# Optimization experiments

Hardware: AMD Instinct MI355X
Metric: run time of the kernel (lower is better)

## Reference

```python
import jax, jax.numpy as jnp
import numpy as np

NEG = -1e6  # masked_softmax fill value from the torch source


def setup_inputs() -> dict:
    key = jax.random.key(0)
    ks = jax.random.split(key, 7)
    B, NQ, NK, D, H = 4, 256, 1024, 256, 256
    queries = jax.random.normal(ks[0], (B, NQ, D), dtype=jnp.float32)
    keys_ = jax.random.normal(ks[1], (B, NK, D), dtype=jnp.float32)
    values = jax.random.normal(ks[2], (B, NK, D), dtype=jnp.float32)
    valid_lens = jax.random.randint(ks[3], (B,), 1, NK + 1, dtype=jnp.int32)
    scale = 1.0 / np.sqrt(D)
    Wq = jax.random.normal(ks[4], (D, H), dtype=jnp.float32) * scale
    Wk = jax.random.normal(ks[5], (D, H), dtype=jnp.float32) * scale
    w_v = jax.random.normal(ks[6], (H,), dtype=jnp.float32) * (1.0 / np.sqrt(H))
    return {"queries": queries, "keys": keys_, "values": values,
            "valid_lens": valid_lens, "Wq": Wq, "Wk": Wk, "w_v": w_v}


def reference(queries, keys, values, valid_lens, Wq, Wk, w_v):
    # projections
    q = jnp.einsum('bqd,dh->bqh', queries, Wq)           # [B,NQ,H]
    k = jnp.einsum('bkd,dh->bkh', keys, Wk)              # [B,NK,H]
    # broadcast-add + tanh + dense(->1): scores [B,NQ,NK]
    features = jnp.tanh(q[:, :, None, :] + k[:, None, :, :])  # [B,NQ,NK,H]
    scores = jnp.einsum('bqkh,h->bqk', features, w_v)
    # masked softmax over last axis with per-batch valid lengths
    nk = keys.shape[1]
    mask = jnp.arange(nk)[None, None, :] < valid_lens[:, None, None]  # [B,1,NK]
    scores = jnp.where(mask, scores, NEG)
    attn = jax.nn.softmax(scores, axis=-1)               # [B,NQ,NK]
    # dropout in eval mode -> identity
    return jnp.einsum('bqk,bkd->bqd', attn, values)      # [B,NQ,D]
```

## Files before the change

### kernel.cpp

```cpp
#include <hip/hip_runtime.h>
#include <math.h>

#define BB 4
#define NQ 256
#define NK 1024
#define DD 256
#define HH 256

#define TM 64
#define TN 64
#define TKK 16
#define NT (DD / TKK)

__global__ __launch_bounds__(256) void proj_exp_kernel(
    const float* __restrict__ Q, const float* __restrict__ K,
    const float* __restrict__ Wq, const float* __restrict__ Wk,
    const int* __restrict__ vlen,
    float* __restrict__ Eq, float* __restrict__ Ek)
{
    const int QTILES = (BB * NQ) / TM;
    int bx = blockIdx.x;
    const float* A; const float* W; float* C; int bm;
    if (bx < QTILES) { A = Q; W = Wq; C = Eq; bm = bx * TM; }
    else {
        int kt = bx - QTILES;
        int b = kt >> 4;
        int lr = (kt & 15) * TM;
        if (lr >= vlen[b]) return;
        A = K; W = Wk; C = Ek; bm = kt * TM;
    }
    int bn = blockIdx.y * TN;

    __shared__ float As[2][TKK][TM + 4];
    __shared__ float Ws[2][TKK][TN + 4];

    int tid = threadIdx.x;
    int ar = tid >> 2, ac4 = tid & 3;
    int wkk = tid >> 4, wc4 = tid & 15;
    int ty = tid >> 4, tx = tid & 15;

    float4 aR = *(const float4*)&A[(size_t)(bm + ar) * DD + ac4 * 4];
    float4 wR = *(const float4*)&W[(size_t)wkk * HH + bn + wc4 * 4];

    float acc[4][4] = {};

    for (int t = 0; t < NT; ++t) {
        int cur = t & 1;
        As[cur][ac4 * 4 + 0][ar] = aR.x;
        As[cur][ac4 * 4 + 1][ar] = aR.y;
        As[cur][ac4 * 4 + 2][ar] = aR.z;
        As[cur][ac4 * 4 + 3][ar] = aR.w;
        *(float4*)&Ws[cur][wkk][wc4 * 4] = wR;
        if (t + 1 < NT) {
            int k0 = (t + 1) * TKK;
            aR = *(const float4*)&A[(size_t)(bm + ar) * DD + k0 + ac4 * 4];
            wR = *(const float4*)&W[(size_t)(k0 + wkk) * HH + bn + wc4 * 4];
        }
        __syncthreads();
#pragma unroll
        for (int kk = 0; kk < TKK; ++kk) {
            float4 a4 = *(const float4*)&As[cur][kk][ty * 4];
            float4 w4 = *(const float4*)&Ws[cur][kk][tx * 4];
            acc[0][0] = fmaf(a4.x, w4.x, acc[0][0]);
            acc[0][1] = fmaf(a4.x, w4.y, acc[0][1]);
            acc[0][2] = fmaf(a4.x, w4.z, acc[0][2]);
            acc[0][3] = fmaf(a4.x, w4.w, acc[0][3]);
            acc[1][0] = fmaf(a4.y, w4.x, acc[1][0]);
            acc[1][1] = fmaf(a4.y, w4.y, acc[1][1]);
            acc[1][2] = fmaf(a4.y, w4.z, acc[1][2]);
            acc[1][3] = fmaf(a4.y, w4.w, acc[1][3]);
            acc[2][0] = fmaf(a4.z, w4.x, acc[2][0]);
            acc[2][1] = fmaf(a4.z, w4.y, acc[2][1]);
            acc[2][2] = fmaf(a4.z, w4.z, acc[2][2]);
            acc[2][3] = fmaf(a4.z, w4.w, acc[2][3]);
            acc[3][0] = fmaf(a4.w, w4.x, acc[3][0]);
            acc[3][1] = fmaf(a4.w, w4.y, acc[3][1]);
            acc[3][2] = fmaf(a4.w, w4.z, acc[3][2]);
            acc[3][3] = fmaf(a4.w, w4.w, acc[3][3]);
        }
        __syncthreads();
    }

#pragma unroll
    for (int i = 0; i < 4; ++i) {
        int m = bm + ty * 4 + i;
        float4 o;
        o.x = __expf(2.f * fminf(fmaxf(acc[i][0], -8.f), 8.f));
        o.y = __expf(2.f * fminf(fmaxf(acc[i][1], -8.f), 8.f));
        o.z = __expf(2.f * fminf(fmaxf(acc[i][2], -8.f), 8.f));
        o.w = __expf(2.f * fminf(fmaxf(acc[i][3], -8.f), 8.f));
        *(float4*)&C[(size_t)m * HH + bn + tx * 4] = o;
    }
}

__global__ __launch_bounds__(256) void scores_kernel(
    const float* __restrict__ Eq, const float* __restrict__ Ek,
    const float* __restrict__ wv, const int* __restrict__ vlen,
    float* __restrict__ P, float* __restrict__ Psum)
{
    __shared__ __align__(16) float sQ[32][HH + 4];
    __shared__ __align__(16) float sK[32][HH + 4];
    __shared__ __align__(16) float sW[HH];

    int bid = blockIdx.x;
    int b = bid & 3;
    int rest = bid >> 2;
    int qc = rest & 7;
    int kc = rest >> 3;
    int L = vlen[b];
    int k0 = kc * 32;
    if (k0 >= L) return;
    int q0 = qc * 32;

    int tid = threadIdx.x;
    {
        int c4 = tid & 63, r0 = tid >> 6;
        const float4* gq = (const float4*)(Eq + ((size_t)b * NQ + q0) * HH);
        const float4* gk = (const float4*)(Ek + ((size_t)b * NK + k0) * HH);
#pragma unroll
        for (int r = 0; r < 32; r += 4) {
            *(float4*)&sQ[r + r0][c4 * 4] = gq[(size_t)(r + r0) * (HH / 4) + c4];
            *(float4*)&sK[r + r0][c4 * 4] = gk[(size_t)(r + r0) * (HH / 4) + c4];
        }
        sW[tid] = wv[tid];
    }
    __syncthreads();

    int ki = tid & 15, qi = tid >> 4;
    float a00 = 0.f, a01 = 0.f, a10 = 0.f, a11 = 0.f;
    const float4* qp0 = (const float4*)&sQ[qi][0];
    const float4* qp1 = (const float4*)&sQ[qi + 16][0];
    const float4* kp0 = (const float4*)&sK[ki][0];
    const float4* kp1 = (const float4*)&sK[ki + 16][0];
    const float4* wp  = (const float4*)sW;

#pragma unroll 4
    for (int h4 = 0; h4 < HH / 4; ++h4) {
        float4 w = wp[h4];
        float wxy = w.x + w.y, wzw = w.z + w.w;
        float4 A0 = qp0[h4], A1 = qp1[h4];
        float4 B0 = kp0[h4], B1 = kp1[h4];
#define QUAD(acc, Aq, Bk)                                                    \
        {                                                                    \
            float E1 = Aq.x * Bk.x, E2 = Aq.y * Bk.y;                        \
            float E3 = Aq.z * Bk.z, E4 = Aq.w * Bk.w;                        \
            float d1 = E1 + 1.f, d2 = E2 + 1.f;                              \
            float d3 = E3 + 1.f, d4 = E4 + 1.f;                              \
            float n12 = fmaf(w.x, E2, fmaf(w.y, E1, wxy));                   \
            float n34 = fmaf(w.z, E4, fmaf(w.w, E3, wzw));                   \
            float d12 = d1 * d2, d34 = d3 * d4;                              \
            float num = fmaf(n12, d34, n34 * d12);                           \
            acc = fmaf(num, __builtin_amdgcn_rcpf(d12 * d34), acc);          \
        }
        QUAD(a00, A0, B0);
        QUAD(a01, A0, B1);
        QUAD(a10, A1, B0);
        QUAD(a11, A1, B1);
#undef QUAD
    }

    int kA = k0 + ki, kB = kA + 16;
    float p00 = (kA < L) ? __expf(-2.f * a00) : 0.f;
    float p10 = (kA < L) ? __expf(-2.f * a10) : 0.f;
    float p01 = (kB < L) ? __expf(-2.f * a01) : 0.f;
    float p11 = (kB < L) ? __expf(-2.f * a11) : 0.f;

    float* s0 = P + ((size_t)b * NQ + q0 + qi) * NK;
    float* s1 = P + ((size_t)b * NQ + q0 + qi + 16) * NK;
    s0[kA] = p00; s0[kB] = p01;
    s1[kA] = p10; s1[kB] = p11;

    float r0s = p00 + p01, r1s = p10 + p11;
#pragma unroll
    for (int o = 1; o <= 8; o <<= 1) {
        r0s += __shfl_xor(r0s, o, 64);
        r1s += __shfl_xor(r1s, o, 64);
    }
    if (ki == 0) {
        Psum[((size_t)b * NQ + q0 + qi) * 32 + kc] = r0s;
        Psum[((size_t)b * NQ + q0 + qi + 16) * 32 + kc] = r1s;
    }
}

__global__ __launch_bounds__(256) void pv_kernel(
    const float* __restrict__ P, const float* __restrict__ V,
    const float* __restrict__ Psum, const int* __restrict__ vlen,
    float* __restrict__ out)
{
    __shared__ __align__(16) float sPt[2][32][36];
    __shared__ __align__(16) float sV[2][32][36];
    __shared__ float sAll[3][64][17];
    __shared__ float sRowsum[32];

    int bid = blockIdx.x;
    int b = bid & 3;
    int rest = bid >> 2;
    int qt = rest >> 3, dt = rest & 7;
    int q0 = qt * 32, d0 = dt * 32;
    int L = vlen[b];
    int nc = (L + 31) >> 5;

    int tid = threadIdx.x;
    if (tid < 32) {
        float s = 0.f;
        const float* pp = Psum + ((size_t)b * NQ + q0 + tid) * 32;
        for (int c = 0; c < nc; ++c) s += pp[c];
        sRowsum[tid] = s;
    }

    int r = tid >> 3, c4 = tid & 7;
    int w = tid >> 6, sp = tid & 63;
    int qg = sp >> 3, dg = sp & 7;

    const float* Pb = P + ((size_t)b * NQ + q0 + r) * NK;
    const float* Vb = V + (size_t)b * NK * DD + d0;

    float4 pf = *(const float4*)(Pb + c4 * 4);
    float4 vf = *(const float4*)(Vb + (size_t)r * DD + c4 * 4);

    float acc[4][4] = {};

    for (int c = 0; c < nc; ++c) {
        int cur = c & 1;
        sPt[cur][c4 * 4 + 0][r] = pf.x;
        sPt[cur][c4 * 4 + 1][r] = pf.y;
        sPt[cur][c4 * 4 + 2][r] = pf.z;
        sPt[cur][c4 * 4 + 3][r] = pf.w;
        *(float4*)&sV[cur][r][c4 * 4] = vf;
        if (c + 1 < nc) {
            int kn = (c + 1) * 32;
            pf = *(const float4*)(Pb + kn + c4 * 4);
            vf = *(const float4*)(Vb + (size_t)(kn + r) * DD + c4 * 4);
        }
        __syncthreads();
#pragma unroll
        for (int kk = 0; kk < 8; ++kk) {
            float4 A  = *(const float4*)&sPt[cur][w * 8 + kk][qg * 4];
            float4 Bv = *(const float4*)&sV[cur][w * 8 + kk][dg * 4];
            acc[0][0] = fmaf(A.x, Bv.x, acc[0][0]);
            acc[0][1] = fmaf(A.x, Bv.y, acc[0][1]);
            acc[0][2] = fmaf(A.x, Bv.z, acc[0][2]);
            acc[0][3] = fmaf(A.x, Bv.w, acc[0][3]);
            acc[1][0] = fmaf(A.y, Bv.x, acc[1][0]);
            acc[1][1] = fmaf(A.y, Bv.y, acc[1][1]);
            acc[1][2] = fmaf(A.y, Bv.z, acc[1][2]);
            acc[1][3] = fmaf(A.y, Bv.w, acc[1][3]);
            acc[2][0] = fmaf(A.z, Bv.x, acc[2][0]);
            acc[2][1] = fmaf(A.z, Bv.y, acc[2][1]);
            acc[2][2] = fmaf(A.z, Bv.z, acc[2][2]);
            acc[2][3] = fmaf(A.z, Bv.w, acc[2][3]);
            acc[3][0] = fmaf(A.w, Bv.x, acc[3][0]);
            acc[3][1] = fmaf(A.w, Bv.y, acc[3][1]);
            acc[3][2] = fmaf(A.w, Bv.z, acc[3][2]);
            acc[3][3] = fmaf(A.w, Bv.w, acc[3][3]);
        }
        __syncthreads();
    }

    if (w > 0) {
#pragma unroll
        for (int i = 0; i < 4; ++i)
#pragma unroll
            for (int j = 0; j < 4; ++j) sAll[w - 1][sp][i * 4 + j] = acc[i][j];
    }
    __syncthreads();
    if (w == 0) {
#pragma unroll
        for (int ww = 0; ww < 3; ++ww)
#pragma unroll
            for (int i = 0; i < 4; ++i)
#pragma unroll
                for (int j = 0; j < 4; ++j) acc[i][j] += sAll[ww][sp][i * 4 + j];
#pragma unroll
        for (int i = 0; i < 4; ++i) {
            float inv = 1.0f / sRowsum[qg * 4 + i];
            float4 o = { acc[i][0] * inv, acc[i][1] * inv,
                         acc[i][2] * inv, acc[i][3] * inv };
            *(float4*)&out[((size_t)b * NQ + q0 + qg * 4 + i) * DD + d0 + dg * 4] = o;
        }
    }
}

extern "C" void kernel_launch(void* const* d_in, const int* in_sizes, int n_in,
                              void* d_out, int out_size, void* d_ws, size_t ws_size,
                              hipStream_t stream) {
    const float* queries = (const float*)d_in[0];
    const float* keys    = (const float*)d_in[1];
    const float* values  = (const float*)d_in[2];
    const int*   vlens   = (const int*)d_in[3];
    const float* Wq      = (const float*)d_in[4];
    const float* Wk      = (const float*)d_in[5];
    const float* wv      = (const float*)d_in[6];
    float* out = (float*)d_out;

    float* Eqb  = (float*)d_ws;
    float* Ekb  = Eqb + (size_t)BB * NQ * HH;
    float* P    = Ekb + (size_t)BB * NK * HH;
    float* Psum = P + (size_t)BB * NQ * NK;

    dim3 pgrid((BB * NQ) / TM + (BB * NK) / TM, HH / TN);
    proj_exp_kernel<<<pgrid, 256, 0, stream>>>(queries, keys, Wq, Wk, vlens,
                                               Eqb, Ekb);

    scores_kernel<<<dim3(BB * (NQ / 32) * (NK / 32)), 256, 0, stream>>>(
        Eqb, Ekb, wv, vlens, P, Psum);

    pv_kernel<<<dim3(BB * (NQ / 32) * (DD / 32)), 256, 0, stream>>>(
        P, values, Psum, vlens, out);
}
```

Before: 56.14 us.

## Stream scores-kernel H dimension in double-buffered chunks and drop trailing barriers

The scores kernel no longer stages full 256-wide Q and K rows in shared memory. It streams 64-wide H chunks through a double buffer, prefetching the next chunk into registers while the current one is computed, with a single barrier per chunk. This shrinks LDS use substantially, which should allow more resident blocks and overlap global loads with math. The trailing __syncthreads in the projection and PV GEMM loops is also removed. That saves barriers, but it could introduce shared-memory races if those loops depended on the barrier before overwriting a buffer.

```diff
diff --git a/kernel.cpp b/kernel.cpp
--- a/kernel.cpp
+++ b/kernel.cpp
@@ -78,7 +78,6 @@
             acc[3][2] = fmaf(a4.w, w4.z, acc[3][2]);
             acc[3][3] = fmaf(a4.w, w4.w, acc[3][3]);
         }
-        __syncthreads();
     }
 
 #pragma unroll
@@ -93,13 +92,16 @@
     }
 }
 
+#define HC 64
+#define NHCH (HH / HC)
+
 __global__ __launch_bounds__(256) void scores_kernel(
     const float* __restrict__ Eq, const float* __restrict__ Ek,
     const float* __restrict__ wv, const int* __restrict__ vlen,
     float* __restrict__ P, float* __restrict__ Psum)
 {
-    __shared__ __align__(16) float sQ[32][HH + 4];
-    __shared__ __align__(16) float sK[32][HH + 4];
+    __shared__ __align__(16) float sQ[2][32][HC + 4];
+    __shared__ __align__(16) float sK[2][32][HC + 4];
     __shared__ __align__(16) float sW[HH];
 
     int bid = blockIdx.x;
@@ -113,50 +115,62 @@
     int q0 = qc * 32;
 
     int tid = threadIdx.x;
-    {
-        int c4 = tid & 63, r0 = tid >> 6;
-        const float4* gq = (const float4*)(Eq + ((size_t)b * NQ + q0) * HH);
-        const float4* gk = (const float4*)(Ek + ((size_t)b * NK + k0) * HH);
-#pragma unroll
-        for (int r = 0; r < 32; r += 4) {
-            *(float4*)&sQ[r + r0][c4 * 4] = gq[(size_t)(r + r0) * (HH / 4) + c4];
-            *(float4*)&sK[r + r0][c4 * 4] = gk[(size_t)(r + r0) * (HH / 4) + c4];
-        }
-        sW[tid] = wv[tid];
-    }
-    __syncthreads();
+    int lr = tid >> 3;
+    int lc = tid & 7;
+
+    const float* gq = Eq + ((size_t)b * NQ + q0 + lr) * HH;
+    const float* gk = Ek + ((size_t)b * NK + k0 + lr) * HH;
+
+    float4 q1 = *(const float4*)&gq[lc * 4];
+    float4 q2 = *(const float4*)&gq[lc * 4 + 32];
+    float4 k1 = *(const float4*)&gk[lc * 4];
+    float4 k2 = *(const float4*)&gk[lc * 4 + 32];
+    sW[tid] = wv[tid];
 
     int ki = tid & 15, qi = tid >> 4;
     float a00 = 0.f, a01 = 0.f, a10 = 0.f, a11 = 0.f;
-    const float4* qp0 = (const float4*)&sQ[qi][0];
-    const float4* qp1 = (const float4*)&sQ[qi + 16][0];
-    const float4* kp0 = (const float4*)&sK[ki][0];
-    const float4* kp1 = (const float4*)&sK[ki + 16][0];
-    const float4* wp  = (const float4*)sW;
-
-#pragma unroll 4
-    for (int h4 = 0; h4 < HH / 4; ++h4) {
-        float4 w = wp[h4];
-        float wxy = w.x + w.y, wzw = w.z + w.w;
-        float4 A0 = qp0[h4], A1 = qp1[h4];
-        float4 B0 = kp0[h4], B1 = kp1[h4];
+
+    for (int c = 0; c < NHCH; ++c) {
+        int cur = c & 1;
+        *(float4*)&sQ[cur][lr][lc * 4] = q1;
+        *(float4*)&sQ[cur][lr][lc * 4 + 32] = q2;
+        *(float4*)&sK[cur][lr][lc * 4] = k1;
+        *(float4*)&sK[cur][lr][lc * 4 + 32] = k2;
+        if (c + 1 < NHCH) {
+            int h0 = (c + 1) * HC;
+            q1 = *(const float4*)&gq[h0 + lc * 4];
+            q2 = *(const float4*)&gq[h0 + lc * 4 + 32];
+            k1 = *(const float4*)&gk[h0 + lc * 4];
+            k2 = *(const float4*)&gk[h0 + lc * 4 + 32];
+        }
+        __syncthreads();
+
+#pragma unroll
+        for (int h4 = 0; h4 < HC / 4; ++h4) {
+            float4 w = *(const float4*)&sW[c * HC + h4 * 4];
+            float wxy = w.x + w.y, wzw = w.z + w.w;
+            float4 A0 = *(const float4*)&sQ[cur][qi][h4 * 4];
+            float4 A1 = *(const float4*)&sQ[cur][qi + 16][h4 * 4];
+            float4 B0 = *(const float4*)&sK[cur][ki][h4 * 4];
+            float4 B1 = *(const float4*)&sK[cur][ki + 16][h4 * 4];
 #define QUAD(acc, Aq, Bk)                                                    \
-        {                                                                    \
-            float E1 = Aq.x * Bk.x, E2 = Aq.y * Bk.y;                        \
-            float E3 = Aq.z * Bk.z, E4 = Aq.w * Bk.w;                        \
-            float d1 = E1 + 1.f, d2 = E2 + 1.f;                              \
-            float d3 = E3 + 1.f, d4 = E4 + 1.f;                              \
-            float n12 = fmaf(w.x, E2, fmaf(w.y, E1, wxy));                   \
-            float n34 = fmaf(w.z, E4, fmaf(w.w, E3, wzw));                   \
-            float d12 = d1 * d2, d34 = d3 * d4;                              \
-            float num = fmaf(n12, d34, n34 * d12);                           \
-            acc = fmaf(num, __builtin_amdgcn_rcpf(d12 * d34), acc);          \
-        }
-        QUAD(a00, A0, B0);
-        QUAD(a01, A0, B1);
-        QUAD(a10, A1, B0);
-        QUAD(a11, A1, B1);
+            {                                                                \
+                float E1 = Aq.x * Bk.x, E2 = Aq.y * Bk.y;                    \
+                float E3 = Aq.z * Bk.z, E4 = Aq.w * Bk.w;                    \
+                float d1 = E1 + 1.f, d2 = E2 + 1.f;                          \
+                float d3 = E3 + 1.f, d4 = E4 + 1.f;                          \
+                float n12 = fmaf(w.x, E2, fmaf(w.y, E1, wxy));               \
+                float n34 = fmaf(w.z, E4, fmaf(w.w, E3, wzw));               \
+                float d12 = d1 * d2, d34 = d3 * d4;                          \
+                float num = fmaf(n12, d34, n34 * d12);                       \
+                acc = fmaf(num, __builtin_amdgcn_rcpf(d12 * d34), acc);      \
+            }
+            QUAD(a00, A0, B0);
+            QUAD(a01, A0, B1);
+            QUAD(a10, A1, B0);
+            QUAD(a11, A1, B1);
 #undef QUAD
+        }
     }
 
     int kA = k0 + ki, kB = kA + 16;
@@ -254,7 +268,6 @@
             acc[3][2] = fmaf(A.w, Bv.z, acc[3][2]);
             acc[3][3] = fmaf(A.w, Bv.w, acc[3][3]);
         }
-        __syncthreads();
     }
 
     if (w > 0) {
```

Result: slower. 58.23 us (+3.7%).

## Shrink projection tiles, drop redundant barriers, deepen PV register prefetch

Applied to the files above, without the earlier changes.

The projection kernel moves from 64x64 to 32x64 output tiles on a flattened 1D grid. This produces more blocks and finer skipping of masked key rows, but only half the threads load A. The trailing __syncthreads in both the projection and PV main loops is removed, on the basis that double-buffered shared memory needs only one barrier per iteration. The PV kernel now prefetches two chunks ahead into alternating register sets to hide global-load latency, at the cost of more registers and some branching.

```diff
diff --git a/kernel.cpp b/kernel.cpp
--- a/kernel.cpp
+++ b/kernel.cpp
@@ -7,8 +7,8 @@
 #define DD 256
 #define HH 256
 
-#define TM 64
-#define TN 64
+#define TMR 32
+#define TNC 64
 #define TKK 16
 #define NT (DD / TKK)
 
@@ -18,72 +18,68 @@
     const int* __restrict__ vlen,
     float* __restrict__ Eq, float* __restrict__ Ek)
 {
-    const int QTILES = (BB * NQ) / TM;
+    const int QROWT = (BB * NQ) / TMR;
     int bx = blockIdx.x;
+    int rt = bx >> 2, ct = bx & 3;
     const float* A; const float* W; float* C; int bm;
-    if (bx < QTILES) { A = Q; W = Wq; C = Eq; bm = bx * TM; }
+    if (rt < QROWT) { A = Q; W = Wq; C = Eq; bm = rt * TMR; }
     else {
-        int kt = bx - QTILES;
-        int b = kt >> 4;
-        int lr = (kt & 15) * TM;
+        int kt = rt - QROWT;
+        int b = kt >> 5;
+        int lr = (kt & 31) * TMR;
         if (lr >= vlen[b]) return;
-        A = K; W = Wk; C = Ek; bm = kt * TM;
-    }
-    int bn = blockIdx.y * TN;
-
-    __shared__ float As[2][TKK][TM + 4];
-    __shared__ float Ws[2][TKK][TN + 4];
+        A = K; W = Wk; C = Ek; bm = kt * TMR;
+    }
+    int bn = ct * TNC;
+
+    __shared__ float As[2][TKK][TMR + 2];
+    __shared__ float Ws[2][TKK][TNC + 4];
 
     int tid = threadIdx.x;
-    int ar = tid >> 2, ac4 = tid & 3;
+    int ar = (tid >> 2) & 31, ac4 = tid & 3;
     int wkk = tid >> 4, wc4 = tid & 15;
     int ty = tid >> 4, tx = tid & 15;
 
-    float4 aR = *(const float4*)&A[(size_t)(bm + ar) * DD + ac4 * 4];
-    float4 wR = *(const float4*)&W[(size_t)wkk * HH + bn + wc4 * 4];
-
-    float acc[4][4] = {};
+    float4 aR = {0,0,0,0}, wR;
+    if (tid < 128) aR = *(const float4*)&A[(size_t)(bm + ar) * DD + ac4 * 4];
+    wR = *(const float4*)&W[(size_t)wkk * HH + bn + wc4 * 4];
+
+    float acc[2][4] = {};
 
     for (int t = 0; t < NT; ++t) {
         int cur = t & 1;
-        As[cur][ac4 * 4 + 0][ar] = aR.x;
-        As[cur][ac4 * 4 + 1][ar] = aR.y;
-        As[cur][ac4 * 4 + 2][ar] = aR.z;
-        As[cur][ac4 * 4 + 3][ar] = aR.w;
+        if (tid < 128) {
+            As[cur][ac4 * 4 + 0][ar] = aR.x;
+            As[cur][ac4 * 4 + 1][ar] = aR.y;
+            As[cur][ac4 * 4 + 2][ar] = aR.z;
+            As[cur][ac4 * 4 + 3][ar] = aR.w;
+        }
         *(float4*)&Ws[cur][wkk][wc4 * 4] = wR;
         if (t + 1 < NT) {
             int k0 = (t + 1) * TKK;
-            aR = *(const float4*)&A[(size_t)(bm + ar) * DD + k0 + ac4 * 4];
+            if (tid < 128)
+                aR = *(const float4*)&A[(size_t)(bm + ar) * DD + k0 + ac4 * 4];
             wR = *(const float4*)&W[(size_t)(k0 + wkk) * HH + bn + wc4 * 4];
         }
         __syncthreads();
 #pragma unroll
         for (int kk = 0; kk < TKK; ++kk) {
-            float4 a4 = *(const float4*)&As[cur][kk][ty * 4];
+            float2 a2 = *(const float2*)&As[cur][kk][ty * 2];
             float4 w4 = *(const float4*)&Ws[cur][kk][tx * 4];
-            acc[0][0] = fmaf(a4.x, w4.x, acc[0][0]);
-            acc[0][1] = fmaf(a4.x, w4.y, acc[0][1]);
-            acc[0][2] = fmaf(a4.x, w4.z, acc[0][2]);
-            acc[0][3] = fmaf(a4.x, w4.w, acc[0][3]);
-            acc[1][0] = fmaf(a4.y, w4.x, acc[1][0]);
-            acc[1][1] = fmaf(a4.y, w4.y, acc[1][1]);
-            acc[1][2] = fmaf(a4.y, w4.z, acc[1][2]);
-            acc[1][3] = fmaf(a4.y, w4.w, acc[1][3]);
-            acc[2][0] = fmaf(a4.z, w4.x, acc[2][0]);
-            acc[2][1] = fmaf(a4.z, w4.y, acc[2][1]);
-            acc[2][2] = fmaf(a4.z, w4.z, acc[2][2]);
-            acc[2][3] = fmaf(a4.z, w4.w, acc[2][3]);
-            acc[3][0] = fmaf(a4.w, w4.x, acc[3][0]);
-            acc[3][1] = fmaf(a4.w, w4.y, acc[3][1]);
-            acc[3][2] = fmaf(a4.w, w4.z, acc[3][2]);
-            acc[3][3] = fmaf(a4.w, w4.w, acc[3][3]);
-        }
-        __syncthreads();
-    }
-
-#pragma unroll
-    for (int i = 0; i < 4; ++i) {
-        int m = bm + ty * 4 + i;
+            acc[0][0] = fmaf(a2.x, w4.x, acc[0][0]);
+            acc[0][1] = fmaf(a2.x, w4.y, acc[0][1]);
+            acc[0][2] = fmaf(a2.x, w4.z, acc[0][2]);
+            acc[0][3] = fmaf(a2.x, w4.w, acc[0][3]);
+            acc[1][0] = fmaf(a2.y, w4.x, acc[1][0]);
+            acc[1][1] = fmaf(a2.y, w4.y, acc[1][1]);
+            acc[1][2] = fmaf(a2.y, w4.z, acc[1][2]);
+            acc[1][3] = fmaf(a2.y, w4.w, acc[1][3]);
+        }
+    }
+
+#pragma unroll
+    for (int i = 0; i < 2; ++i) {
+        int m = bm + ty * 2 + i;
         float4 o;
         o.x = __expf(2.f * fminf(fmaxf(acc[i][0], -8.f), 8.f));
         o.y = __expf(2.f * fminf(fmaxf(acc[i][1], -8.f), 8.f));
@@ -215,22 +211,38 @@
     const float* Pb = P + ((size_t)b * NQ + q0 + r) * NK;
     const float* Vb = V + (size_t)b * NK * DD + d0;
 
-    float4 pf = *(const float4*)(Pb + c4 * 4);
-    float4 vf = *(const float4*)(Vb + (size_t)r * DD + c4 * 4);
+    float4 pf0 = *(const float4*)(Pb + c4 * 4);
+    float4 vf0 = *(const float4*)(Vb + (size_t)r * DD + c4 * 4);
+    int c1i = (nc > 1) ? 32 : 0;
+    float4 pf1 = *(const float4*)(Pb + c1i + c4 * 4);
+    float4 vf1 = *(const float4*)(Vb + (size_t)(c1i + r) * DD + c4 * 4);
 
     float acc[4][4] = {};
 
     for (int c = 0; c < nc; ++c) {
         int cur = c & 1;
-        sPt[cur][c4 * 4 + 0][r] = pf.x;
-        sPt[cur][c4 * 4 + 1][r] = pf.y;
-        sPt[cur][c4 * 4 + 2][r] = pf.z;
-        sPt[cur][c4 * 4 + 3][r] = pf.w;
-        *(float4*)&sV[cur][r][c4 * 4] = vf;
-        if (c + 1 < nc) {
-            int kn = (c + 1) * 32;
-            pf = *(const float4*)(Pb + kn + c4 * 4);
-            vf = *(const float4*)(Vb + (size_t)(kn + r) * DD + c4 * 4);
+        if (cur == 0) {
+            sPt[0][c4 * 4 + 0][r] = pf0.x;
+            sPt[0][c4 * 4 + 1][r] = pf0.y;
+            sPt[0][c4 * 4 + 2][r] = pf0.z;
+            sPt[0][c4 * 4 + 3][r] = pf0.w;
+            *(float4*)&sV[0][r][c4 * 4] = vf0;
+            if (c + 2 < nc) {
+                int kn = (c + 2) * 32;
+                pf0 = *(const float4*)(Pb + kn + c4 * 4);
+                vf0 = *(const float4*)(Vb + (size_t)(kn + r) * DD + c4 * 4);
+            }
+        } else {
+            sPt[1][c4 * 4 + 0][r] = pf1.x;
+            sPt[1][c4 * 4 + 1][r] = pf1.y;
+            sPt[1][c4 * 4 + 2][r] = pf1.z;
+            sPt[1][c4 * 4 + 3][r] = pf1.w;
+            *(float4*)&sV[1][r][c4 * 4] = vf1;
+            if (c + 2 < nc) {
+                int kn = (c + 2) * 32;
+                pf1 = *(const float4*)(Pb + kn + c4 * 4);
+                vf1 = *(const float4*)(Vb + (size_t)(kn + r) * DD + c4 * 4);
+            }
         }
         __syncthreads();
 #pragma unroll
@@ -254,7 +266,6 @@
             acc[3][2] = fmaf(A.w, Bv.z, acc[3][2]);
             acc[3][3] = fmaf(A.w, Bv.w, acc[3][3]);
         }
-        __syncthreads();
     }
 
     if (w > 0) {
@@ -298,9 +309,8 @@
     float* P    = Ekb + (size_t)BB * NK * HH;
     float* Psum = P + (size_t)BB * NQ * NK;
 
-    dim3 pgrid((BB * NQ) / TM + (BB * NK) / TM, HH / TN);
-    proj_exp_kernel<<<pgrid, 256, 0, stream>>>(queries, keys, Wq, Wk, vlens,
-                                               Eqb, Ekb);
+    proj_exp_kernel<<<dim3(((BB * NQ) / TMR + (BB * NK) / TMR) * 4), 256, 0,
+                      stream>>>(queries, keys, Wq, Wk, vlens, Eqb, Ekb);
 
     scores_kernel<<<dim3(BB * (NQ / 32) * (NK / 32)), 256, 0, stream>>>(
         Eqb, Ekb, wv, vlens, P, Psum);
```

Result: slower. 59.07 us (+5.2%).
